# Optimization experiments

Measured on AMD Instinct MI355X. Metric: run time of the kernel, lower is better.

Reference implementation:

```python
import jax, jax.numpy as jnp
import numpy as np

SEQ_LEN, BATCH, HIDDEN, OUT = 512, 4096, 2048, 10


def setup_inputs() -> dict:
    key = jax.random.key(0)
    ks = jax.random.split(key, 7)
    return {
        "x": jax.random.normal(ks[0], (SEQ_LEN, BATCH), jnp.float32),
        "Wx": jax.random.normal(ks[1], (HIDDEN, 1), jnp.float32) * 0.05,
        "bx": jax.random.normal(ks[2], (HIDDEN,), jnp.float32) * 0.05,
        "Wh": jax.random.normal(ks[3], (1, HIDDEN), jnp.float32) * 0.05,
        "bh": jax.random.normal(ks[4], (1,), jnp.float32) * 0.05,
        "Wy": jax.random.normal(ks[5], (OUT, HIDDEN), jnp.float32) * 0.05,
        "by": jax.random.normal(ks[6], (OUT,), jnp.float32) * 0.05,
    }


def reference(x, Wx, bx, Wh, bh, Wy, by):
    # x: [T, B]; input_dim == 1 structurally (torch code reshapes x[i] to (B, 1)).
    B = x.shape[1]
    H = Wx.shape[0]
    wx = Wx[:, 0]  # [H]

    def step(h, xt):
        # linear_x(x_t): (B,1) @ (1,H) -> outer product, [B, H]
        x_out = xt[:, None] * wx[None, :] + bx
        # linear_h(h): [B, H] @ [H, 1] -> [B, 1], broadcasts into the add (as in torch)
        h_out = h @ Wh.T + bh
        h_new = jnp.tanh(x_out + h_out)
        return h_new, None

    h0 = jnp.zeros((B, H), x.dtype)
    h_final, _ = jax.lax.scan(step, h0, x)
    logits = h_final @ Wy.T + by  # [B, OUT]
    return jax.nn.softmax(logits, axis=-1)
```

## Files before the change

kernel.cpp:

```cpp
#include <hip/hip_runtime.h>
#include <math.h>


#define SEQ   512
#define BATCH 4096
#define HID   2048
#define NOUT  10
#define KPL   32
#define NS    560
#define ROWQ  9

#define S_LOc   (-10.0f)
#define S_H     (20.0f / 559.0f)
#define S_INVH  (559.0f / 20.0f)
#define S_BIAS  (10.0f * S_INVH)
#define NSM1F   559.0f
#define NSM4F   556.0f
#define U_SCALE (8.0f / 14.0f)
#define U_BIAS  4.0f
#define UCMAXF  7.99951f

#define TABLE_FLOATS (NS * ROWQ * 4)
#define WSA_FLOATS (4096 + 14 * 4096)
#define WSB_FLOATS (4096 + 4 * 4096)
#define DZ14 43.0f
#define DZ9  69.875f

__device__ __forceinline__ float fast_exp2(float v) { return __builtin_amdgcn_exp2f(v); }
__device__ __forceinline__ float fast_rcp(float v)  { return __builtin_amdgcn_rcpf(v); }
__device__ __forceinline__ float fast_tanh(float a) {
    const float C = 2.8853900817779268f;
    return __builtin_fmaf(-2.0f, fast_rcp(fast_exp2(C * a) + 1.0f), 1.0f);
}
__device__ __forceinline__ float wave_sum(float v) {
#pragma unroll
    for (int m = 1; m < 64; m <<= 1) v += __shfl_xor(v, m, 64);
    return v;
}
__device__ __forceinline__ float combine_eval(float z255, int nn, float dz,
                                              const float* baseA, const float* baseB,
                                              int split, int b) {
    float p = z255 / dz;
    int   c = min(max((int)floorf(p) - 1, 0), nn - 4);
    float t = p - (float)c;
    float a0 = t, a1 = t - 1.0f, a2 = t - 2.0f, a3 = t - 3.0f;
    float m01 = a0 * a1, m23 = a2 * a3;
    float w0 = a1 * m23 * (-1.0f / 6.0f), w1 = a0 * m23 * 0.5f;
    float w2 = m01 * a3 * (-0.5f),        w3 = m01 * a2 * (1.0f / 6.0f);
    float y[4];
#pragma unroll
    for (int i = 0; i < 4; ++i) {
        int n = c + i;
        const float* ptr = (n < split) ? (baseA + (size_t)n * 4096)
                                       : (baseB + (size_t)(n - split) * 4096);
        y[i] = ptr[b];
    }
    return __builtin_fmaf(w0, y[0], w1 * y[1]) + __builtin_fmaf(w2, y[2], w3 * y[3]);
}

__global__ __launch_bounds__(256) void k_coef(const float* __restrict__ Wx, const float* __restrict__ bx,
                                              const float* __restrict__ Wh, const float* __restrict__ bh,
                                              float* __restrict__ tab_g) {
    __shared__ float red[256];
    __shared__ float Gn[32];
    const int k    = blockIdx.x;
    const int node = threadIdx.x & 31;
    const int jc   = threadIdx.x >> 5;
    const int cell = node >> 2, nn = node & 3;
    const float sn = S_LOc + (float)k * S_H;
    const float xi_n = (nn == 0) ? 0.923879533f : (nn == 1) ? 0.382683432f
                     : (nn == 2) ? -0.382683432f : -0.923879533f;
    const float un = (-7.0f + ((float)cell + 0.5f) * 1.75f) + 0.875f * xi_n;
    float p = 0.0f;
    const int j0 = jc * 256;
#pragma unroll 4
    for (int j = j0; j < j0 + 256; ++j)
        p += Wh[j] * fast_tanh(__builtin_fmaf(Wx[j], un, bx[j] + sn));
    red[threadIdx.x] = p;
    __syncthreads();
    if (threadIdx.x < 32) {
        float V = bh[0];
#pragma unroll
        for (int c = 0; c < 8; ++c) V += red[threadIdx.x + 32 * c];
        Gn[threadIdx.x] = __builtin_fmaf(V, S_INVH, S_BIAS);
    }
    __syncthreads();
    float4* wq = (float4*)tab_g;
    if (threadIdx.x < 8) {
        const int c = threadIdx.x;
        float G0 = Gn[4*c+0], G1 = Gn[4*c+1], G2 = Gn[4*c+2], G3 = Gn[4*c+3];
        float d03 = G0 - G3, d12 = G1 - G2;
        float a0 = 0.25f * (G0 + G1 + G2 + G3);
        float a1 = 0.5f * (0.923879533f * d03 + 0.382683432f * d12);
        float a2 = 0.5f * 0.707106781f * (G0 - G1 - G2 + G3);
        float a3 = 0.5f * (0.382683432f * d03 - 0.923879533f * d12);
        wq[k * ROWQ + c] = make_float4(a0 - a2, a1 - 3.0f * a3, 2.0f * a2, 4.0f * a3);
    } else if (threadIdx.x == 8) {
        wq[k * ROWQ + 8] = make_float4(0.f, 0.f, 0.f, 0.f);
    }
}

__global__ __launch_bounds__(256) void k_scan_seg(const float* __restrict__ x,
                                                  const float* __restrict__ bh,
                                                  const float* __restrict__ tab_g,
                                                  float* __restrict__ z255,
                                                  float* __restrict__ baseA,
                                                  float* __restrict__ baseB,
                                                  int split, float dz) {
    __shared__ float4 tabs[5200];
    {
        const float4* src = (const float4*)tab_g;
        for (int i = threadIdx.x; i < NS * ROWQ; i += 256) tabs[i] = src[i];
    }
    __syncthreads();
    const int blk = blockIdx.x;
    const int seg  = (blk < 16) ? 0 : 1;
    const int node = seg ? (blk - 16) >> 4 : 0;
    const int eb   = seg ? (blk - 16) & 15 : blk;
    const int b    = eb * 256 + threadIdx.x;

    const int t0     = seg ? 255 : 0;
    const int nsteps = seg ? 256 : 255;

    float z = seg ? (float)node * dz
                  : fminf(fmaxf(__builtin_fmaf(bh[0], S_INVH, S_BIAS), 0.0f), NSM1F);

    auto step1 = [&](float u) {
        float uc = fminf(fmaxf(__builtin_fmaf(u, U_SCALE, U_BIAS), 0.0f), UCMAXF);
        float cf = floorf(uc);
        float xi = __builtin_fmaf(2.0f, uc - cf, -1.0f);
        int   ci = (int)cf;
        float zc  = fminf(fmaxf(z, 0.0f), NSM1F);
        float kzf = fminf(fmaxf(floorf(zc) - 1.0f, 0.0f), NSM4F);
        int   kzi = (int)kzf;
        float ts  = zc - kzf;
        float c0 = ts, c1 = ts - 1.0f, c2 = ts - 2.0f, c3 = ts - 3.0f;
        float n01 = c0 * c1, n23 = c2 * c3;
        float ws0 = c1 * n23 * (-1.0f / 6.0f), ws1 = c0 * n23 * 0.5f;
        float ws2 = n01 * c3 * (-0.5f),        ws3 = n01 * c2 * (1.0f / 6.0f);
        const int base = kzi * ROWQ + ci;
        float4 q0 = tabs[base];
        float4 q1 = tabs[base + ROWQ];
        float4 q2 = tabs[base + 2 * ROWQ];
        float4 q3 = tabs[base + 3 * ROWQ];
        float r0 = __builtin_fmaf(__builtin_fmaf(__builtin_fmaf(q0.w, xi, q0.z), xi, q0.y), xi, q0.x);
        float r1 = __builtin_fmaf(__builtin_fmaf(__builtin_fmaf(q1.w, xi, q1.z), xi, q1.y), xi, q1.x);
        float r2 = __builtin_fmaf(__builtin_fmaf(__builtin_fmaf(q2.w, xi, q2.z), xi, q2.y), xi, q2.x);
        float r3 = __builtin_fmaf(__builtin_fmaf(__builtin_fmaf(q3.w, xi, q3.z), xi, q3.y), xi, q3.x);
        z = __builtin_fmaf(ws0, r0, ws1 * r1) + __builtin_fmaf(ws2, r2, ws3 * r3);
    };

    float cur[8], nxt[8];
#pragma unroll
    for (int i = 0; i < 8; ++i)
        cur[i] = x[(size_t)min(t0 + i, SEQ - 1) * BATCH + b];

    const int full = nsteps >> 3, tail = nsteps & 7;
    for (int c = 0; c < full; ++c) {
        const int nb = t0 + (c + 1) * 8;
#pragma unroll
        for (int i = 0; i < 8; ++i)
            nxt[i] = x[(size_t)min(nb + i, SEQ - 1) * BATCH + b];
#pragma unroll
        for (int i = 0; i < 8; ++i) step1(cur[i]);
#pragma unroll
        for (int i = 0; i < 8; ++i) cur[i] = nxt[i];
    }
    for (int i = 0; i < tail; ++i) step1(cur[i]);

    if (seg == 0) z255[b] = z;
    else {
        float* p = (node < split) ? (baseA + (size_t)node * 4096)
                                  : (baseB + (size_t)(node - split) * 4096);
        p[b] = z;
    }
}

__global__ __launch_bounds__(256) void k_combine(const float* __restrict__ baseA,
                                                 const float* __restrict__ baseB,
                                                 int split, int nn, float dz,
                                                 float* __restrict__ zs) {
    const int b = blockIdx.x * 256 + threadIdx.x;
    float zz = combine_eval(zs[b], nn, dz, baseA, baseB, split, b);
    zs[b] = __builtin_fmaf(zz, S_H, S_LOc);
}

__global__ __launch_bounds__(256) void head_combine_A(
    const float* __restrict__ x,  const float* __restrict__ Wx,
    const float* __restrict__ bx, const float* __restrict__ Wy,
    const float* __restrict__ by, const float* __restrict__ ws,
    float* __restrict__ out)
{
    const int lane = threadIdx.x & 63;
    const int wave = threadIdx.x >> 6;
    const int b    = blockIdx.x * 4 + wave;

    float zz = combine_eval(ws[b], 14, DZ14, ws + 4096, ws + 4096, 14, b);
    const float s = __builtin_fmaf(zz, S_H, S_LOc);

    const float C  = 2.8853900817779268f;
    const float u  = x[(size_t)(SEQ - 1) * BATCH + b];
    const float sc = s * C;
    float acc[NOUT];
#pragma unroll
    for (int i = 0; i < NOUT; ++i) acc[i] = 0.0f;
#pragma unroll 4
    for (int k = 0; k < KPL; ++k) {
        const int j = k * 64 + lane;
        float arg = __builtin_fmaf(u, Wx[j] * C, bx[j] * C) + sc;
        float r   = fast_rcp(fast_exp2(arg) + 1.0f);
        float th  = __builtin_fmaf(-2.0f, r, 1.0f);
#pragma unroll
        for (int i = 0; i < NOUT; ++i)
            acc[i] = __builtin_fmaf(Wy[i * HID + j], th, acc[i]);
    }
#pragma unroll
    for (int i = 0; i < NOUT; ++i) acc[i] = wave_sum(acc[i]) + by[i];
    float m = acc[0];
#pragma unroll
    for (int i = 1; i < NOUT; ++i) m = fmaxf(m, acc[i]);
    const float L2E = 1.4426950408889634f;
    float ev[NOUT]; float Z = 0.0f;
#pragma unroll
    for (int i = 0; i < NOUT; ++i) { ev[i] = fast_exp2((acc[i] - m) * L2E); Z += ev[i]; }
    const float rz = fast_rcp(Z);
    if (lane == 0) {
#pragma unroll
        for (int i = 0; i < NOUT; ++i) out[(size_t)b * NOUT + i] = ev[i] * rz;
    }
}

__global__ __launch_bounds__(256) void rnn_scan_exact(
    const float* __restrict__ x,  const float* __restrict__ Wx,
    const float* __restrict__ bx, const float* __restrict__ Wh,
    const float* __restrict__ bh, float* __restrict__ s_out)
{
    const int lane = threadIdx.x & 63;
    const int wave = threadIdx.x >> 6;
    const int b    = blockIdx.x * 4 + wave;
    const float C = 2.8853900817779268f;
    float wxs[KPL], bxs[KPL], whn[KPL];
    float swh = 0.0f;
#pragma unroll
    for (int k = 0; k < KPL; ++k) {
        const int j = k * 64 + lane;
        const float w = Wh[j];
        wxs[k] = Wx[j] * C; bxs[k] = bx[j] * C; whn[k] = -2.0f * w; swh += w;
    }
    swh = wave_sum(swh);
    const float bh0 = bh[0];
    const float K0  = bh0 + swh;
    float s = bh0, u = x[b];
    for (int t = 0; t < SEQ - 1; ++t) {
        float u_next = x[(size_t)(t + 1) * BATCH + b];
        const float sc = s * C;
        float p = 0.0f;
#pragma unroll
        for (int k = 0; k < KPL; ++k) {
            float arg = __builtin_fmaf(u, wxs[k], bxs[k]) + sc;
            float r   = fast_rcp(fast_exp2(arg) + 1.0f);
            p = __builtin_fmaf(whn[k], r, p);
        }
        s = K0 + wave_sum(p);
        u = u_next;
    }
    if (lane == 0) s_out[b] = s;
}

__global__ __launch_bounds__(256) void rnn_head_exact(
    const float* __restrict__ x,  const float* __restrict__ Wx,
    const float* __restrict__ bx, const float* __restrict__ Wy,
    const float* __restrict__ by, const float* __restrict__ s_in,
    float* __restrict__ out)
{
    const int lane = threadIdx.x & 63;
    const int wave = threadIdx.x >> 6;
    const int b    = blockIdx.x * 4 + wave;
    const float C  = 2.8853900817779268f;
    const float s  = s_in[b];
    const float u  = x[(size_t)(SEQ - 1) * BATCH + b];
    const float sc = s * C;
    float acc[NOUT];
#pragma unroll
    for (int i = 0; i < NOUT; ++i) acc[i] = 0.0f;
#pragma unroll 4
    for (int k = 0; k < KPL; ++k) {
        const int j = k * 64 + lane;
        float arg = __builtin_fmaf(u, Wx[j] * C, bx[j] * C) + sc;
        float r   = fast_rcp(fast_exp2(arg) + 1.0f);
        float th  = __builtin_fmaf(-2.0f, r, 1.0f);
#pragma unroll
        for (int i = 0; i < NOUT; ++i)
            acc[i] = __builtin_fmaf(Wy[i * HID + j], th, acc[i]);
    }
#pragma unroll
    for (int i = 0; i < NOUT; ++i) acc[i] = wave_sum(acc[i]) + by[i];
    float m = acc[0];
#pragma unroll
    for (int i = 1; i < NOUT; ++i) m = fmaxf(m, acc[i]);
    const float L2E = 1.4426950408889634f;
    float ev[NOUT]; float Z = 0.0f;
#pragma unroll
    for (int i = 0; i < NOUT; ++i) { ev[i] = fast_exp2((acc[i] - m) * L2E); Z += ev[i]; }
    const float rz = fast_rcp(Z);
    if (lane == 0) {
#pragma unroll
        for (int i = 0; i < NOUT; ++i) out[(size_t)b * NOUT + i] = ev[i] * rz;
    }
}

extern "C" void kernel_launch(void* const* d_in, const int* in_sizes, int n_in,
                              void* d_out, int out_size, void* d_ws, size_t ws_size,
                              hipStream_t stream)
{
    const float* x  = (const float*)d_in[0];
    const float* Wx = (const float*)d_in[1];
    const float* bx = (const float*)d_in[2];
    const float* Wh = (const float*)d_in[3];
    const float* bh = (const float*)d_in[4];
    const float* Wy = (const float*)d_in[5];
    const float* by = (const float*)d_in[6];
    float* out = (float*)d_out;
    float* wf  = (float*)d_ws;

    if (ws_size >= (size_t)WSA_FLOATS * sizeof(float)) {
        k_coef<<<NS, 256, 0, stream>>>(Wx, bx, Wh, bh, out);
        k_scan_seg<<<16 + 14 * 16, 256, 0, stream>>>(x, bh, out, wf,
                                                     wf + 4096, wf + 4096, 14, DZ14);
        head_combine_A<<<BATCH / 4, 256, 0, stream>>>(x, Wx, bx, Wy, by, wf, out);
    } else if (ws_size >= (size_t)WSB_FLOATS * sizeof(float)) {
        k_coef<<<NS, 256, 0, stream>>>(Wx, bx, Wh, bh, out);
        k_scan_seg<<<16 + 9 * 16, 256, 0, stream>>>(x, bh, out, wf,
                                                    out + TABLE_FLOATS, wf + 4096, 5, DZ9);
        k_combine<<<16, 256, 0, stream>>>(out + TABLE_FLOATS, wf + 4096, 5, 9, DZ9, wf);
        rnn_head_exact<<<BATCH / 4, 256, 0, stream>>>(x, Wx, bx, Wy, by, wf, out);
    } else {
        rnn_scan_exact<<<BATCH / 4, 256, 0, stream>>>(x, Wx, bx, Wh, bh, wf);
        rnn_head_exact<<<BATCH / 4, 256, 0, stream>>>(x, Wx, bx, Wy, by, wf, out);
    }
}
```

Baseline: 144.0 us.

## Fuse coefficient, segmented scan and head kernels into one persistent kernel with grid barriers

Replaces the three-launch path (table build, segmented scan, combine+softmax head) with a single persistent kernel of 240 blocks that separates the phases with atomic-counter grid barriers. The barrier counters live in the output buffer and are zeroed by a memset before launch. The aim is to remove launch gaps and inter-kernel drains. In exchange, the table phase and the head phase now run on only 240 blocks, which lowers parallelism there, and the barriers rely on all blocks being co-resident.

```diff
diff --git a/kernel.cpp b/kernel.cpp
--- a/kernel.cpp
+++ b/kernel.cpp
@@ -9,6 +9,7 @@
 #define KPL   32
 #define NS    560
 #define ROWQ  9
+#define NB    240
 
 #define S_LOc   (-10.0f)
 #define S_H     (20.0f / 559.0f)
@@ -21,8 +22,9 @@
 #define UCMAXF  7.99951f
 
 #define TABLE_FLOATS (NS * ROWQ * 4)
-#define WSA_FLOATS (4096 + 14 * 4096)
-#define WSB_FLOATS (4096 + 4 * 4096)
+#define CNT_IDX      40952
+#define WSA_FLOATS   (4096 + 14 * 4096)
+#define WSB_FLOATS   (4096 + 4 * 4096)
 #define DZ14 43.0f
 #define DZ9  69.875f
 
@@ -37,6 +39,192 @@
     for (int m = 1; m < 64; m <<= 1) v += __shfl_xor(v, m, 64);
     return v;
 }
+
+__device__ __forceinline__ void grid_barrier(unsigned* cnt) {
+    __syncthreads();
+    if (threadIdx.x == 0) {
+        __threadfence();
+        __hip_atomic_fetch_add(cnt, 1u, __ATOMIC_ACQ_REL, __HIP_MEMORY_SCOPE_AGENT);
+        unsigned v;
+        do {
+            __builtin_amdgcn_s_sleep(8);
+            v = __hip_atomic_load(cnt, __ATOMIC_ACQUIRE, __HIP_MEMORY_SCOPE_AGENT);
+        } while (v < (unsigned)NB);
+        __threadfence();
+    }
+    __syncthreads();
+}
+
+__device__ __forceinline__ float combine14(float z255, const float* nodes, int e) {
+    float p = z255 * (1.0f / DZ14);
+    int   c = min(max((int)floorf(p) - 1, 0), 10);
+    float t = p - (float)c;
+    float a0 = t, a1 = t - 1.0f, a2 = t - 2.0f, a3 = t - 3.0f;
+    float m01 = a0 * a1, m23 = a2 * a3;
+    float w0 = a1 * m23 * (-1.0f / 6.0f), w1 = a0 * m23 * 0.5f;
+    float w2 = m01 * a3 * (-0.5f),        w3 = m01 * a2 * (1.0f / 6.0f);
+    float y0 = nodes[(size_t)c * 4096 + e];
+    float y1 = nodes[(size_t)(c + 1) * 4096 + e];
+    float y2 = nodes[(size_t)(c + 2) * 4096 + e];
+    float y3 = nodes[(size_t)(c + 3) * 4096 + e];
+    return __builtin_fmaf(w0, y0, w1 * y1) + __builtin_fmaf(w2, y2, w3 * y3);
+}
+
+__global__ __launch_bounds__(256) void k_fused(
+    const float* __restrict__ x,  const float* __restrict__ Wx,
+    const float* __restrict__ bx, const float* __restrict__ Wh,
+    const float* __restrict__ bh, const float* __restrict__ Wy,
+    const float* __restrict__ by, float* __restrict__ out,
+    float* __restrict__ ws)
+{
+    __shared__ float4 tabs[5200];
+    float* scr = (float*)tabs;
+    const int blk = blockIdx.x, tid = threadIdx.x;
+    unsigned* cnt = (unsigned*)(out + CNT_IDX);
+    float* tab_g = out;
+
+    {
+        const int node = tid & 31, jc = tid >> 5;
+        const int cell = node >> 2, nn = node & 3;
+        const float xi_n = (nn == 0) ? 0.923879533f : (nn == 1) ? 0.382683432f
+                         : (nn == 2) ? -0.382683432f : -0.923879533f;
+        const float un = (-7.0f + ((float)cell + 0.5f) * 1.75f) + 0.875f * xi_n;
+        for (int r = blk; r < NS; r += NB) {
+            const float sn = S_LOc + (float)r * S_H;
+            float p = 0.0f;
+            const int j0 = jc * 256;
+#pragma unroll 4
+            for (int j = j0; j < j0 + 256; ++j)
+                p += Wh[j] * fast_tanh(__builtin_fmaf(Wx[j], un, bx[j] + sn));
+            scr[tid] = p;
+            __syncthreads();
+            if (tid < 32) {
+                float V = bh[0];
+#pragma unroll
+                for (int c = 0; c < 8; ++c) V += scr[tid + 32 * c];
+                scr[256 + tid] = __builtin_fmaf(V, S_INVH, S_BIAS);
+            }
+            __syncthreads();
+            if (tid < 8) {
+                const int c = tid;
+                float G0 = scr[256 + 4*c], G1 = scr[257 + 4*c], G2 = scr[258 + 4*c], G3 = scr[259 + 4*c];
+                float d03 = G0 - G3, d12 = G1 - G2;
+                float a0 = 0.25f * (G0 + G1 + G2 + G3);
+                float a1 = 0.5f * (0.923879533f * d03 + 0.382683432f * d12);
+                float a2 = 0.5f * 0.707106781f * (G0 - G1 - G2 + G3);
+                float a3 = 0.5f * (0.382683432f * d03 - 0.923879533f * d12);
+                ((float4*)tab_g)[r * ROWQ + c] =
+                    make_float4(a0 - a2, a1 - 3.0f * a3, 2.0f * a2, 4.0f * a3);
+            } else if (tid == 8) {
+                ((float4*)tab_g)[r * ROWQ + 8] = make_float4(0.f, 0.f, 0.f, 0.f);
+            }
+            __syncthreads();
+        }
+    }
+    grid_barrier(cnt);
+
+    {
+        const float4* src = (const float4*)tab_g;
+        for (int i = tid; i < NS * ROWQ; i += 256) tabs[i] = src[i];
+        __syncthreads();
+
+        const int seg  = (blk < 16) ? 0 : 1;
+        const int node = seg ? (blk - 16) >> 4 : 0;
+        const int eb   = seg ? (blk - 16) & 15 : blk;
+        const int b    = eb * 256 + tid;
+        const int t0     = seg ? 255 : 0;
+        const int nsteps = seg ? 256 : 255;
+
+        float z = seg ? (float)node * DZ14
+                      : fminf(fmaxf(__builtin_fmaf(bh[0], S_INVH, S_BIAS), 0.0f), NSM1F);
+
+        auto step1 = [&](float u) {
+            float uc = fminf(fmaxf(__builtin_fmaf(u, U_SCALE, U_BIAS), 0.0f), UCMAXF);
+            float cf = floorf(uc);
+            float xi = __builtin_fmaf(2.0f, uc - cf, -1.0f);
+            int   ci = (int)cf;
+            float zc  = fminf(fmaxf(z, 0.0f), NSM1F);
+            float kzf = fminf(fmaxf(floorf(zc) - 1.0f, 0.0f), NSM4F);
+            int   kzi = (int)kzf;
+            float ts  = zc - kzf;
+            float c0 = ts, c1 = ts - 1.0f, c2 = ts - 2.0f, c3 = ts - 3.0f;
+            float n01 = c0 * c1, n23 = c2 * c3;
+            float ws0 = c1 * n23 * (-1.0f / 6.0f), ws1 = c0 * n23 * 0.5f;
+            float ws2 = n01 * c3 * (-0.5f),        ws3 = n01 * c2 * (1.0f / 6.0f);
+            const int base = kzi * ROWQ + ci;
+            float4 q0 = tabs[base];
+            float4 q1 = tabs[base + ROWQ];
+            float4 q2 = tabs[base + 2 * ROWQ];
+            float4 q3 = tabs[base + 3 * ROWQ];
+            float r0 = __builtin_fmaf(__builtin_fmaf(__builtin_fmaf(q0.w, xi, q0.z), xi, q0.y), xi, q0.x);
+            float r1 = __builtin_fmaf(__builtin_fmaf(__builtin_fmaf(q1.w, xi, q1.z), xi, q1.y), xi, q1.x);
+            float r2 = __builtin_fmaf(__builtin_fmaf(__builtin_fmaf(q2.w, xi, q2.z), xi, q2.y), xi, q2.x);
+            float r3 = __builtin_fmaf(__builtin_fmaf(__builtin_fmaf(q3.w, xi, q3.z), xi, q3.y), xi, q3.x);
+            z = __builtin_fmaf(ws0, r0, ws1 * r1) + __builtin_fmaf(ws2, r2, ws3 * r3);
+        };
+
+        float cur[8], nxt[8];
+#pragma unroll
+        for (int i = 0; i < 8; ++i)
+            cur[i] = x[(size_t)min(t0 + i, SEQ - 1) * BATCH + b];
+        const int full = nsteps >> 3, tail = nsteps & 7;
+        for (int c = 0; c < full; ++c) {
+            const int nb = t0 + (c + 1) * 8;
+#pragma unroll
+            for (int i = 0; i < 8; ++i)
+                nxt[i] = x[(size_t)min(nb + i, SEQ - 1) * BATCH + b];
+#pragma unroll
+            for (int i = 0; i < 8; ++i) step1(cur[i]);
+#pragma unroll
+            for (int i = 0; i < 8; ++i) cur[i] = nxt[i];
+        }
+        for (int i = 0; i < tail; ++i) step1(cur[i]);
+
+        if (seg == 0) ws[b] = z;
+        else ws[4096 + (size_t)node * 4096 + b] = z;
+    }
+    grid_barrier(cnt + 1);
+
+    {
+        const int lane = tid & 63;
+        const int gw   = blk * 4 + (tid >> 6);
+        const float C  = 2.8853900817779268f;
+        const float L2E = 1.4426950408889634f;
+        for (int e = gw; e < BATCH; e += NB * 4) {
+            float zz = combine14(ws[e], ws + 4096, e);
+            const float s  = __builtin_fmaf(zz, S_H, S_LOc);
+            const float u  = x[(size_t)(SEQ - 1) * BATCH + e];
+            const float sc = s * C;
+            float acc[NOUT];
+#pragma unroll
+            for (int i = 0; i < NOUT; ++i) acc[i] = 0.0f;
+#pragma unroll 4
+            for (int k = 0; k < KPL; ++k) {
+                const int j = k * 64 + lane;
+                float arg = __builtin_fmaf(u, Wx[j] * C, bx[j] * C) + sc;
+                float r   = fast_rcp(fast_exp2(arg) + 1.0f);
+                float th  = __builtin_fmaf(-2.0f, r, 1.0f);
+#pragma unroll
+                for (int i = 0; i < NOUT; ++i)
+                    acc[i] = __builtin_fmaf(Wy[i * HID + j], th, acc[i]);
+            }
+#pragma unroll
+            for (int i = 0; i < NOUT; ++i) acc[i] = wave_sum(acc[i]) + by[i];
+            float m = acc[0];
+#pragma unroll
+            for (int i = 1; i < NOUT; ++i) m = fmaxf(m, acc[i]);
+            float ev[NOUT]; float Z = 0.0f;
+#pragma unroll
+            for (int i = 0; i < NOUT; ++i) { ev[i] = fast_exp2((acc[i] - m) * L2E); Z += ev[i]; }
+            const float rz = fast_rcp(Z);
+            if (lane == 0) {
+#pragma unroll
+                for (int i = 0; i < NOUT; ++i) out[(size_t)e * NOUT + i] = ev[i] * rz;
+            }
+        }
+    }
+}
+
 __device__ __forceinline__ float combine_eval(float z255, int nn, float dz,
                                               const float* baseA, const float* baseB,
                                               int split, int b) {
@@ -64,8 +252,7 @@
     __shared__ float red[256];
     __shared__ float Gn[32];
     const int k    = blockIdx.x;
-    const int node = threadIdx.x & 31;
-    const int jc   = threadIdx.x >> 5;
+    const int node = threadIdx.x & 31, jc = threadIdx.x >> 5;
     const int cell = node >> 2, nn = node & 3;
     const float sn = S_LOc + (float)k * S_H;
     const float xi_n = (nn == 0) ? 0.923879533f : (nn == 1) ? 0.382683432f
@@ -118,13 +305,10 @@
     const int node = seg ? (blk - 16) >> 4 : 0;
     const int eb   = seg ? (blk - 16) & 15 : blk;
     const int b    = eb * 256 + threadIdx.x;
-
     const int t0     = seg ? 255 : 0;
     const int nsteps = seg ? 256 : 255;
-
     float z = seg ? (float)node * dz
                   : fminf(fmaxf(__builtin_fmaf(bh[0], S_INVH, S_BIAS), 0.0f), NSM1F);
-
     auto step1 = [&](float u) {
         float uc = fminf(fmaxf(__builtin_fmaf(u, U_SCALE, U_BIAS), 0.0f), UCMAXF);
         float cf = floorf(uc);
@@ -149,12 +333,10 @@
         float r3 = __builtin_fmaf(__builtin_fmaf(__builtin_fmaf(q3.w, xi, q3.z), xi, q3.y), xi, q3.x);
         z = __builtin_fmaf(ws0, r0, ws1 * r1) + __builtin_fmaf(ws2, r2, ws3 * r3);
     };
-
     float cur[8], nxt[8];
 #pragma unroll
     for (int i = 0; i < 8; ++i)
         cur[i] = x[(size_t)min(t0 + i, SEQ - 1) * BATCH + b];
-
     const int full = nsteps >> 3, tail = nsteps & 7;
     for (int c = 0; c < full; ++c) {
         const int nb = t0 + (c + 1) * 8;
@@ -167,7 +349,6 @@
         for (int i = 0; i < 8; ++i) cur[i] = nxt[i];
     }
     for (int i = 0; i < tail; ++i) step1(cur[i]);
-
     if (seg == 0) z255[b] = z;
     else {
         float* p = (node < split) ? (baseA + (size_t)node * 4096)
@@ -183,51 +364,6 @@
     const int b = blockIdx.x * 256 + threadIdx.x;
     float zz = combine_eval(zs[b], nn, dz, baseA, baseB, split, b);
     zs[b] = __builtin_fmaf(zz, S_H, S_LOc);
-}
-
-__global__ __launch_bounds__(256) void head_combine_A(
-    const float* __restrict__ x,  const float* __restrict__ Wx,
-    const float* __restrict__ bx, const float* __restrict__ Wy,
-    const float* __restrict__ by, const float* __restrict__ ws,
-    float* __restrict__ out)
-{
-    const int lane = threadIdx.x & 63;
-    const int wave = threadIdx.x >> 6;
-    const int b    = blockIdx.x * 4 + wave;
-
-    float zz = combine_eval(ws[b], 14, DZ14, ws + 4096, ws + 4096, 14, b);
-    const float s = __builtin_fmaf(zz, S_H, S_LOc);
-
-    const float C  = 2.8853900817779268f;
-    const float u  = x[(size_t)(SEQ - 1) * BATCH + b];
-    const float sc = s * C;
-    float acc[NOUT];
-#pragma unroll
-    for (int i = 0; i < NOUT; ++i) acc[i] = 0.0f;
-#pragma unroll 4
-    for (int k = 0; k < KPL; ++k) {
-        const int j = k * 64 + lane;
-        float arg = __builtin_fmaf(u, Wx[j] * C, bx[j] * C) + sc;
-        float r   = fast_rcp(fast_exp2(arg) + 1.0f);
-        float th  = __builtin_fmaf(-2.0f, r, 1.0f);
-#pragma unroll
-        for (int i = 0; i < NOUT; ++i)
-            acc[i] = __builtin_fmaf(Wy[i * HID + j], th, acc[i]);
-    }
-#pragma unroll
-    for (int i = 0; i < NOUT; ++i) acc[i] = wave_sum(acc[i]) + by[i];
-    float m = acc[0];
-#pragma unroll
-    for (int i = 1; i < NOUT; ++i) m = fmaxf(m, acc[i]);
-    const float L2E = 1.4426950408889634f;
-    float ev[NOUT]; float Z = 0.0f;
-#pragma unroll
-    for (int i = 0; i < NOUT; ++i) { ev[i] = fast_exp2((acc[i] - m) * L2E); Z += ev[i]; }
-    const float rz = fast_rcp(Z);
-    if (lane == 0) {
-#pragma unroll
-        for (int i = 0; i < NOUT; ++i) out[(size_t)b * NOUT + i] = ev[i] * rz;
-    }
 }
 
 __global__ __launch_bounds__(256) void rnn_scan_exact(
@@ -324,10 +460,8 @@
     float* wf  = (float*)d_ws;
 
     if (ws_size >= (size_t)WSA_FLOATS * sizeof(float)) {
-        k_coef<<<NS, 256, 0, stream>>>(Wx, bx, Wh, bh, out);
-        k_scan_seg<<<16 + 14 * 16, 256, 0, stream>>>(x, bh, out, wf,
-                                                     wf + 4096, wf + 4096, 14, DZ14);
-        head_combine_A<<<BATCH / 4, 256, 0, stream>>>(x, Wx, bx, Wy, by, wf, out);
+        hipMemsetAsync(out + CNT_IDX, 0, 2 * sizeof(unsigned), stream);
+        k_fused<<<NB, 256, 0, stream>>>(x, Wx, bx, Wh, bh, Wy, by, out, wf);
     } else if (ws_size >= (size_t)WSB_FLOATS * sizeof(float)) {
         k_coef<<<NS, 256, 0, stream>>>(Wx, bx, Wh, bh, out);
         k_scan_seg<<<16 + 9 * 16, 256, 0, stream>>>(x, bh, out, wf,
```

Measured after the change: 204.0 us. 1.42x slower.
